# Optimization experiments

Hardware: AMD Instinct MI355X
Metric: run time of the kernel (lower is better)

The kernel has to match this reference:

```python
import jax, jax.numpy as jnp
import numpy as np
import functools

N_NODES = 16
WIDTH = 64
C_DIM = 3
LATENT_DIM = 8
B = 131072


def build_graph(n=N_NODES, k=4, p=0.75, seed=0):
    """Watts-Strogatz-style random graph oriented low->high node id (DAG),
    mirroring build_random_graph(nodes, 1 input, 1 output, p=0.75, k=4)."""
    rng = np.random.RandomState(seed)
    edges = set()
    for i in range(n):
        for d in range(1, k // 2 + 1):
            j = (i + d) % n
            if rng.rand() < p:
                j = int(rng.randint(n))
            a, b = min(i, j), max(i, j)
            if a != b:
                edges.add((a, b))
    preds = [set() for _ in range(n)]
    for a, b in edges:
        preds[b].add(a)
    # every non-source node must have a predecessor (connectivity)
    for j in range(1, n):
        if not preds[j]:
            a = int(rng.randint(j))
            preds[j].add(a)
            edges.add((a, j))
    succs = [set() for _ in range(n)]
    for a, b in edges:
        succs[a].add(b)
    preds = [sorted(p_) for p_ in preds]
    sources = [j for j in range(n) if not preds[j]]   # receive the INR feature f
    sinks = [j for j in range(n) if not succs[j]]     # combined into the single output
    return preds, sources, sinks


def gaussian(x):
    return jnp.exp(-0.5 * x * x)

# 'large' activation set for graph nodes, assigned deterministically per node
GRAPH_ACTS = [jnp.tanh, jax.nn.elu, jax.nn.softplus, jnp.sin, gaussian]


def setup_inputs() -> dict:
    key = jax.random.key(0)
    ks = jax.random.split(key, 16)

    def nrm(k, shape, s):
        return jax.random.normal(k, shape, dtype=jnp.float32) * s

    inputs = jax.random.normal(ks[0], (B, 3, 1), dtype=jnp.float32)   # (x, y, r) coords
    latents = jax.random.normal(ks[1], (B, LATENT_DIM), dtype=jnp.float32)
    Wl = nrm(ks[2], (WIDTH, LATENT_DIM), 0.3)
    bl = jnp.zeros((WIDTH,), jnp.float32)
    Wx = nrm(ks[3], (WIDTH, 1), 1.0)
    Wy = nrm(ks[4], (WIDTH, 1), 1.0)
    Wr = nrm(ks[5], (WIDTH, 1), 1.0)
    W1 = nrm(ks[6], (WIDTH, WIDTH), 0.15)
    b1 = jnp.zeros((WIDTH,), jnp.float32)
    gW = nrm(ks[7], (N_NODES, WIDTH, WIDTH), 0.15)   # per-graph-node Linear(width,width)
    gB = jnp.zeros((N_NODES, WIDTH), jnp.float32)
    outW = nrm(ks[8], (C_DIM, WIDTH), 0.15)          # combine -> c_dim output
    outb = jnp.zeros((C_DIM,), jnp.float32)
    scale = jnp.ones((1,), jnp.float32)              # ScaleAct learnable scalar
    return {"inputs": inputs, "latents": latents, "Wl": Wl, "bl": bl, "Wx": Wx,
            "Wy": Wy, "Wr": Wr, "W1": W1, "b1": b1, "gW": gW, "gB": gB,
            "outW": outW, "outb": outb, "scale": scale}


def reference(inputs, latents, Wl, bl, Wx, Wy, Wr, W1, b1, gW, gB, outW, outb, scale):
    x, y, r = inputs[:, 0, :], inputs[:, 1, :], inputs[:, 2, :]   # each (B, 1)
    latents_ = jnp.tanh(latents @ Wl.T + bl)      # acts_start[0] = Tanh
    r_ = jax.nn.elu(r @ Wr.T)                     # acts_start[1] = ELU
    y_ = jax.nn.softplus(y @ Wy.T)                # acts_start[2] = Softplus
    x_ = jnp.tanh(x @ Wx.T)                       # acts_start[3] = Tanh
    f = gaussian(x_ + y_ + r_ + latents_)         # acts_start[4] = Gaussian
    f = jnp.sin(f @ W1.T + b1)                    # acts_start[5] = SinLayer

    # random-topology graph network: gather(sum preds) -> linear -> activation
    preds, sources, sinks = build_graph()
    hs = []
    for j in range(N_NODES):
        if j in sources:
            inp = f
        else:
            inp = functools.reduce(lambda a, b_: a + b_, [hs[i] for i in preds[j]])
        hs.append(GRAPH_ACTS[j % len(GRAPH_ACTS)](inp @ gW[j].T + gB[j]))
    agg = functools.reduce(lambda a, b_: a + b_, [hs[j] for j in sinks])
    res = (agg @ outW.T + outb) * scale           # combine + ScaleAct
    return jax.nn.sigmoid(res)                    # final_activation='sigmoid'
```

## Files before the change

### kernel.cpp

```cpp
#include <hip/hip_runtime.h>
#include <cstdint>

#define NN 16
#define W64 64
#define MT 64
#define NSTAGE 17
#define IST 72
#define WST 68

typedef _Float16 half8   __attribute__((ext_vector_type(8)));
typedef _Float16 half16  __attribute__((ext_vector_type(16)));
typedef float    floatx4 __attribute__((ext_vector_type(4)));

struct GPlan {
    unsigned pred[NN];
    unsigned sinkmask;
    int slot[NSTAGE];
    int nslot;
};

constexpr unsigned mt_next(unsigned (&mt)[624], int &mti) {
    if (mti >= 624) {
        for (int i = 0; i < 624; ++i) {
            const unsigned y = (mt[i] & 0x80000000u) | (mt[(i + 1) % 624] & 0x7fffffffu);
            unsigned v = mt[(i + 397) % 624] ^ (y >> 1);
            if (y & 1u) v ^= 0x9908b0dfu;
            mt[i] = v;
        }
        mti = 0;
    }
    unsigned y = mt[mti++];
    y ^= y >> 11;
    y ^= (y << 7)  & 0x9d2c5680u;
    y ^= (y << 15) & 0xefc60000u;
    y ^= y >> 18;
    return y;
}
constexpr double mt_rnd(unsigned (&mt)[624], int &mti) {
    const unsigned a = mt_next(mt, mti) >> 5;
    const unsigned b = mt_next(mt, mti) >> 6;
    return (a * 67108864.0 + b) / 9007199254740992.0;
}
constexpr long mt_randint(unsigned (&mt)[624], int &mti, long n) {
    const unsigned long maxv = (unsigned long)n - 1;
    if (maxv == 0) return 0;
    unsigned long mask = maxv;
    mask |= mask >> 1;  mask |= mask >> 2;  mask |= mask >> 4;
    mask |= mask >> 8;  mask |= mask >> 16;
    unsigned long v = (unsigned long)mt_next(mt, mti) & mask;
    while (v > maxv) v = (unsigned long)mt_next(mt, mti) & mask;
    return (long)v;
}

constexpr GPlan build_plan() {
    GPlan P = {};
    unsigned mt[624] = {};
    mt[0] = 0u;
    for (int i = 1; i < 624; ++i)
        mt[i] = 1812433253u * (mt[i-1] ^ (mt[i-1] >> 30)) + (unsigned)i;
    int mti = 624;

    bool edge[NN][NN] = {};
    for (int i = 0; i < NN; ++i) {
        for (int d = 1; d <= 2; ++d) {
            int j = (i + d) & (NN - 1);
            if (mt_rnd(mt, mti) < 0.75) j = (int)mt_randint(mt, mti, NN);
            const int a = i < j ? i : j;
            const int b = i < j ? j : i;
            if (a != b) edge[a][b] = true;
        }
    }
    for (int a = 0; a < NN; ++a)
        for (int b = 0; b < NN; ++b)
            if (edge[a][b]) P.pred[b] |= 1u << a;
    for (int j = 1; j < NN; ++j) {
        if (!P.pred[j]) {
            const int a = (int)mt_randint(mt, mti, j);
            P.pred[j] |= 1u << a;
            edge[a][j] = true;
        }
    }
    unsigned succ[NN] = {};
    for (int a = 0; a < NN; ++a)
        for (int b = 0; b < NN; ++b)
            if (edge[a][b]) succ[a] |= 1u << b;
    for (int j = 0; j < NN; ++j)
        if (!succ[j]) P.sinkmask |= 1u << j;

    int lastuse[NSTAGE] = {};
    for (int v = 0; v < NSTAGE; ++v) lastuse[v] = -1;
    for (int j = 0; j < NN; ++j) {
        const unsigned pm = P.pred[j];
        if (pm == 0u) { if (j > lastuse[16]) lastuse[16] = j; }
        else for (int i = 0; i < NN; ++i)
            if (pm & (1u << i)) { if (j > lastuse[i]) lastuse[i] = j; }
    }
    for (int i = 0; i < NN; ++i)
        if (P.sinkmask & (1u << i)) lastuse[i] = 17;

    int defstage[NSTAGE] = {};
    for (int i = 0; i < NN; ++i) defstage[i] = i + 1;
    defstage[16] = 0;

    int nmax = 0;
    for (int s = 0; s <= 16; ++s) {
        const int w = (s == 0) ? 16 : (s - 1);
        bool busy[NSTAGE] = {};
        for (int v = 0; v < NSTAGE; ++v) {
            if (v == w) continue;
            if (defstage[v] < s && lastuse[v] >= s)
                busy[P.slot[v]] = true;
        }
        int k = 0;
        while (busy[k]) ++k;
        P.slot[w] = k;
        if (k + 1 > nmax) nmax = k + 1;
    }
    P.nslot = nmax;
    return P;
}

constexpr GPlan kPlan = build_plan();
constexpr int NSLOT = kPlan.nslot;

__device__ __forceinline__ float act_tanh(float x)     { return 1.0f - 2.0f / (1.0f + __expf(2.0f * x)); }
__device__ __forceinline__ float act_elu(float x)      { return x > 0.0f ? x : __expf(x) - 1.0f; }
__device__ __forceinline__ float act_softplus(float x) { return fmaxf(x, 0.0f) + __logf(1.0f + __expf(-fabsf(x))); }
__device__ __forceinline__ float act_gauss(float x)    { return __expf(-0.5f * x * x); }

__device__ __forceinline__ float apply_act(int a, float x) {
    switch (a) {
        case 0:  return act_tanh(x);
        case 1:  return act_elu(x);
        case 2:  return act_softplus(x);
        case 3:  return __sinf(x);
        default: return act_gauss(x);
    }
}

__device__ __forceinline__ half8 cvt8(float4 a, float4 b) {
    half8 h;
    h[0]=(_Float16)a.x; h[1]=(_Float16)a.y; h[2]=(_Float16)a.z; h[3]=(_Float16)a.w;
    h[4]=(_Float16)b.x; h[5]=(_Float16)b.y; h[6]=(_Float16)b.z; h[7]=(_Float16)b.w;
    return h;
}

__global__ void convert_weights(const float* __restrict__ W1,
                                const float* __restrict__ gW,
                                _Float16* __restrict__ ws)
{
    const int i = blockIdx.x * 256 + threadIdx.x;
    if (i >= NSTAGE * 4096) return;
    const float v = (i < 4096) ? W1[i] : gW[i - 4096];
    ws[i] = (_Float16)v;
}

template<bool F16W>
__global__ __launch_bounds__(256, 3) void inr_mfma_kernel(
    const float* __restrict__ inputs, const float* __restrict__ latents,
    const float* __restrict__ Wl, const float* __restrict__ bl,
    const float* __restrict__ Wx, const float* __restrict__ Wy,
    const float* __restrict__ Wr, const float* __restrict__ W1,
    const float* __restrict__ b1, const float* __restrict__ gW,
    const float* __restrict__ gB, const float* __restrict__ outW,
    const float* __restrict__ outb, const float* __restrict__ scale,
    const _Float16* __restrict__ wsW,
    float* __restrict__ out, int Btot)
{
    __shared__ __align__(16) _Float16 inpbuf[2][MT * IST];
    __shared__ __align__(16) _Float16 wbuf[W64 * WST];

    const int tid  = threadIdx.x;
    const int lane = tid & 63;
    const int wv   = tid >> 6;
    const int q    = lane >> 4;
    const int c    = lane & 15;
    const int rowbase = wv * 16;
    const int m0   = blockIdx.x * MT;

    const int srow = tid >> 3;
    const int sc8  = tid & 7;

    half16 hreg[NSLOT];

    {
        const int em = tid >> 2, ep = tid & 3;
        int mg = m0 + em; if (mg >= Btot) mg = Btot - 1;
        const float x = inputs[mg * 3 + 0];
        const float y = inputs[mg * 3 + 1];
        const float r = inputs[mg * 3 + 2];
        const float4 l0 = *(const float4*)(latents + mg * 8);
        const float4 l1 = *(const float4*)(latents + mg * 8 + 4);
        #pragma unroll
        for (int i = 0; i < 16; ++i) {
            const int k = ep * 16 + i;
            const float4 a = *(const float4*)(Wl + k * 8);
            const float4 b = *(const float4*)(Wl + k * 8 + 4);
            float ld = bl[k];
            ld = fmaf(l0.x, a.x, ld); ld = fmaf(l0.y, a.y, ld);
            ld = fmaf(l0.z, a.z, ld); ld = fmaf(l0.w, a.w, ld);
            ld = fmaf(l1.x, b.x, ld); ld = fmaf(l1.y, b.y, ld);
            ld = fmaf(l1.z, b.z, ld); ld = fmaf(l1.w, b.w, ld);
            const float tk = act_tanh(x * Wx[k]) + act_softplus(y * Wy[k])
                           + act_elu(r * Wr[k]) + act_tanh(ld);
            inpbuf[0][em * IST + k] = (_Float16)act_gauss(tk);
        }
    }
    if constexpr (F16W) {
        const uint4* src = (const uint4*)wsW;
        const uint4 h0 = src[tid], h1 = src[tid + 256];
        *(uint4*)&wbuf[srow * WST + sc8 * 8]        = h0;
        *(uint4*)&wbuf[(srow + 32) * WST + sc8 * 8] = h1;
    } else {
        const float4* src = (const float4*)W1;
        const float4 f0 = src[2 * tid],       f1 = src[2 * tid + 1];
        const float4 f2 = src[2 * tid + 512], f3 = src[2 * tid + 513];
        *(half8*)&wbuf[srow * WST + sc8 * 8]        = cvt8(f0, f1);
        *(half8*)&wbuf[(srow + 32) * WST + sc8 * 8] = cvt8(f2, f3);
    }
    __syncthreads();

    #pragma unroll
    for (int s = 0; s < NSTAGE; ++s) {
        const int slot = s & 1;

        uint4  nh0 = {}, nh1 = {};
        float4 nf0 = {}, nf1 = {}, nf2 = {}, nf3 = {};
        if (s + 1 < NSTAGE) {
            if constexpr (F16W) {
                const uint4* src = (const uint4*)(wsW + (s + 1) * 4096);
                nh0 = src[tid]; nh1 = src[tid + 256];
            } else {
                const float4* src = (const float4*)(gW + s * 4096);
                nf0 = src[2 * tid];       nf1 = src[2 * tid + 1];
                nf2 = src[2 * tid + 512]; nf3 = src[2 * tid + 513];
            }
        }

        const half8 a0 = *(const half8*)&inpbuf[slot][(rowbase + c) * IST +  0 + q * 8];
        const half8 a1 = *(const half8*)&inpbuf[slot][(rowbase + c) * IST + 32 + q * 8];

        const float* bias = (s == 0) ? b1 : (gB + (s - 1) * W64);
        floatx4 acc[4];
        #pragma unroll
        for (int t = 0; t < 4; ++t) {
            const half8 b0  = *(const half8*)&wbuf[(t * 16 + c) * WST +  0 + q * 8];
            const half8 b1f = *(const half8*)&wbuf[(t * 16 + c) * WST + 32 + q * 8];
            const float bs = bias[t * 16 + c];
            floatx4 z = {bs, bs, bs, bs};
            z = __builtin_amdgcn_mfma_f32_16x16x32_f16(a0, b0, z, 0, 0, 0);
            z = __builtin_amdgcn_mfma_f32_16x16x32_f16(a1, b1f, z, 0, 0, 0);
            acc[t] = z;
        }

        const int an    = (s == 0) ? 3 : ((s - 1) % 5);
        const int hslot = kPlan.slot[(s == 0) ? 16 : (s - 1)];
        #pragma unroll
        for (int t = 0; t < 4; ++t) {
            #pragma unroll
            for (int r = 0; r < 4; ++r) {
                const float v = apply_act(an, acc[t][r]);
                hreg[hslot][t * 4 + r] = (_Float16)v;
            }
        }

        if (s + 1 < NSTAGE) {
            const unsigned pm = kPlan.pred[s];
            half16 sum;
            if (pm == 0u) {
                sum = hreg[kPlan.slot[16]];
            } else {
                #pragma unroll
                for (int v = 0; v < 16; ++v) sum[v] = (_Float16)0.0f;
                #pragma unroll
                for (int i = 0; i < NN; ++i) {
                    if (pm & (1u << i)) {
                        sum += hreg[kPlan.slot[i]];
                    }
                }
            }
            const int wslot = (s + 1) & 1;
            #pragma unroll
            for (int t = 0; t < 4; ++t)
                #pragma unroll
                for (int r = 0; r < 4; ++r)
                    inpbuf[wslot][(rowbase + q * 4 + r) * IST + t * 16 + c] =
                        sum[t * 4 + r];

            __syncthreads();
            if constexpr (F16W) {
                *(uint4*)&wbuf[srow * WST + sc8 * 8]        = nh0;
                *(uint4*)&wbuf[(srow + 32) * WST + sc8 * 8] = nh1;
            } else {
                *(half8*)&wbuf[srow * WST + sc8 * 8]        = cvt8(nf0, nf1);
                *(half8*)&wbuf[(srow + 32) * WST + sc8 * 8] = cvt8(nf2, nf3);
            }
            __syncthreads();
        }
    }

    {
        half16 sum;
        #pragma unroll
        for (int v = 0; v < 16; ++v) sum[v] = (_Float16)0.0f;
        #pragma unroll
        for (int j = 0; j < NN; ++j) {
            if (kPlan.sinkmask & (1u << j)) {
                sum += hreg[kPlan.slot[j]];
            }
        }
        #pragma unroll
        for (int t = 0; t < 4; ++t)
            #pragma unroll
            for (int r = 0; r < 4; ++r)
                inpbuf[1][(rowbase + q * 4 + r) * IST + t * 16 + c] = sum[t * 4 + r];
    }
    {
        const int em = tid >> 2, ep = tid & 3;
        float p0 = 0.f, p1 = 0.f, p2 = 0.f;
        #pragma unroll
        for (int h = 0; h < 2; ++h) {
            const half8 hv = *(const half8*)&inpbuf[1][em * IST + ep * 16 + h * 8];
            #pragma unroll
            for (int i = 0; i < 8; ++i) {
                const float av = (float)hv[i];
                const int k = ep * 16 + h * 8 + i;
                p0 = fmaf(av, outW[0 * W64 + k], p0);
                p1 = fmaf(av, outW[1 * W64 + k], p1);
                p2 = fmaf(av, outW[2 * W64 + k], p2);
            }
        }
        p0 += __shfl_xor(p0, 1); p0 += __shfl_xor(p0, 2);
        p1 += __shfl_xor(p1, 1); p1 += __shfl_xor(p1, 2);
        p2 += __shfl_xor(p2, 1); p2 += __shfl_xor(p2, 2);
        const int mg = m0 + em;
        if (ep < 3 && mg < Btot) {
            const float pr = (ep == 0) ? p0 : ((ep == 1) ? p1 : p2);
            const float res = (pr + outb[ep]) * scale[0];
            out[mg * 3 + ep] = 1.0f / (1.0f + __expf(-res));
        }
    }
}

extern "C" void kernel_launch(void* const* d_in, const int* in_sizes, int n_in,
                              void* d_out, int out_size, void* d_ws, size_t ws_size,
                              hipStream_t stream)
{
    const float* inputs  = (const float*)d_in[0];
    const float* latents = (const float*)d_in[1];
    const float* Wl      = (const float*)d_in[2];
    const float* bl      = (const float*)d_in[3];
    const float* Wx      = (const float*)d_in[4];
    const float* Wy      = (const float*)d_in[5];
    const float* Wr      = (const float*)d_in[6];
    const float* W1      = (const float*)d_in[7];
    const float* b1      = (const float*)d_in[8];
    const float* gW      = (const float*)d_in[9];
    const float* gB      = (const float*)d_in[10];
    const float* outW    = (const float*)d_in[11];
    const float* outb    = (const float*)d_in[12];
    const float* scale   = (const float*)d_in[13];
    float* out = (float*)d_out;

    const int Btot = in_sizes[0] / 3;
    const int blocks = (Btot + MT - 1) / MT;
    const size_t wbytes = (size_t)NSTAGE * 4096 * sizeof(_Float16);

    if (ws_size >= wbytes) {
        _Float16* wsW = (_Float16*)d_ws;
        convert_weights<<<(NSTAGE * 4096 + 255) / 256, 256, 0, stream>>>(W1, gW, wsW);
        inr_mfma_kernel<true><<<blocks, 256, 0, stream>>>(
            inputs, latents, Wl, bl, Wx, Wy, Wr, W1, b1, gW, gB, outW, outb, scale,
            wsW, out, Btot);
    } else {
        inr_mfma_kernel<false><<<blocks, 256, 0, stream>>>(
            inputs, latents, Wl, bl, Wx, Wy, Wr, W1, b1, gW, gB, outW, outb, scale,
            (const _Float16*)nullptr, out, Btot);
    }
}
```

Measured before the change: 181.3 us.

## Transpose MFMA operands and read weights from global to drop block barriers

```diff
diff --git a/kernel.cpp b/kernel.cpp
--- a/kernel.cpp
+++ b/kernel.cpp
@@ -6,11 +6,12 @@
 #define MT 64
 #define NSTAGE 17
 #define IST 72
-#define WST 68
-
+
+typedef _Float16 half4   __attribute__((ext_vector_type(4)));
 typedef _Float16 half8   __attribute__((ext_vector_type(8)));
 typedef _Float16 half16  __attribute__((ext_vector_type(16)));
 typedef float    floatx4 __attribute__((ext_vector_type(4)));
+typedef unsigned int uint2v __attribute__((ext_vector_type(2)));
 
 struct GPlan {
     unsigned pred[NN];
@@ -156,7 +157,7 @@
 }
 
 template<bool F16W>
-__global__ __launch_bounds__(256, 3) void inr_mfma_kernel(
+__global__ __launch_bounds__(256, 4) void inr_mfma_kernel(
     const float* __restrict__ inputs, const float* __restrict__ latents,
     const float* __restrict__ Wl, const float* __restrict__ bl,
     const float* __restrict__ Wx, const float* __restrict__ Wy,
@@ -167,8 +168,7 @@
     const _Float16* __restrict__ wsW,
     float* __restrict__ out, int Btot)
 {
-    __shared__ __align__(16) _Float16 inpbuf[2][MT * IST];
-    __shared__ __align__(16) _Float16 wbuf[W64 * WST];
+    __shared__ __align__(16) _Float16 inpbuf[MT * IST];
 
     const int tid  = threadIdx.x;
     const int lane = tid & 63;
@@ -177,9 +177,6 @@
     const int c    = lane & 15;
     const int rowbase = wv * 16;
     const int m0   = blockIdx.x * MT;
-
-    const int srow = tid >> 3;
-    const int sc8  = tid & 7;
 
     half16 hreg[NSLOT];
 
@@ -191,6 +188,7 @@
         const float r = inputs[mg * 3 + 2];
         const float4 l0 = *(const float4*)(latents + mg * 8);
         const float4 l1 = *(const float4*)(latents + mg * 8 + 4);
+        half8 hlo, hhi;
         #pragma unroll
         for (int i = 0; i < 16; ++i) {
             const int k = ep * 16 + i;
@@ -203,53 +201,38 @@
             ld = fmaf(l1.z, b.z, ld); ld = fmaf(l1.w, b.w, ld);
             const float tk = act_tanh(x * Wx[k]) + act_softplus(y * Wy[k])
                            + act_elu(r * Wr[k]) + act_tanh(ld);
-            inpbuf[0][em * IST + k] = (_Float16)act_gauss(tk);
-        }
-    }
-    if constexpr (F16W) {
-        const uint4* src = (const uint4*)wsW;
-        const uint4 h0 = src[tid], h1 = src[tid + 256];
-        *(uint4*)&wbuf[srow * WST + sc8 * 8]        = h0;
-        *(uint4*)&wbuf[(srow + 32) * WST + sc8 * 8] = h1;
-    } else {
-        const float4* src = (const float4*)W1;
-        const float4 f0 = src[2 * tid],       f1 = src[2 * tid + 1];
-        const float4 f2 = src[2 * tid + 512], f3 = src[2 * tid + 513];
-        *(half8*)&wbuf[srow * WST + sc8 * 8]        = cvt8(f0, f1);
-        *(half8*)&wbuf[(srow + 32) * WST + sc8 * 8] = cvt8(f2, f3);
-    }
-    __syncthreads();
+            const _Float16 hv = (_Float16)act_gauss(tk);
+            if (i < 8) hlo[i] = hv; else hhi[i - 8] = hv;
+        }
+        *(half8*)&inpbuf[em * IST + ep * 16]     = hlo;
+        *(half8*)&inpbuf[em * IST + ep * 16 + 8] = hhi;
+    }
 
     #pragma unroll
     for (int s = 0; s < NSTAGE; ++s) {
-        const int slot = s & 1;
-
-        uint4  nh0 = {}, nh1 = {};
-        float4 nf0 = {}, nf1 = {}, nf2 = {}, nf3 = {};
-        if (s + 1 < NSTAGE) {
+        const half8 i0 = *(const half8*)&inpbuf[(rowbase + c) * IST +  0 + q * 8];
+        const half8 i1 = *(const half8*)&inpbuf[(rowbase + c) * IST + 32 + q * 8];
+
+        const float* bias = (s == 0) ? b1 : (gB + (s - 1) * W64);
+
+        floatx4 acc[4];
+        #pragma unroll
+        for (int t = 0; t < 4; ++t) {
+            half8 wlo, whi;
             if constexpr (F16W) {
-                const uint4* src = (const uint4*)(wsW + (s + 1) * 4096);
-                nh0 = src[tid]; nh1 = src[tid + 256];
+                const _Float16* wr = wsW + s * 4096 + (t * 16 + c) * 64 + q * 8;
+                wlo = *(const half8*)wr;
+                whi = *(const half8*)(wr + 32);
             } else {
-                const float4* src = (const float4*)(gW + s * 4096);
-                nf0 = src[2 * tid];       nf1 = src[2 * tid + 1];
-                nf2 = src[2 * tid + 512]; nf3 = src[2 * tid + 513];
-            }
-        }
-
-        const half8 a0 = *(const half8*)&inpbuf[slot][(rowbase + c) * IST +  0 + q * 8];
-        const half8 a1 = *(const half8*)&inpbuf[slot][(rowbase + c) * IST + 32 + q * 8];
-
-        const float* bias = (s == 0) ? b1 : (gB + (s - 1) * W64);
-        floatx4 acc[4];
-        #pragma unroll
-        for (int t = 0; t < 4; ++t) {
-            const half8 b0  = *(const half8*)&wbuf[(t * 16 + c) * WST +  0 + q * 8];
-            const half8 b1f = *(const half8*)&wbuf[(t * 16 + c) * WST + 32 + q * 8];
-            const float bs = bias[t * 16 + c];
-            floatx4 z = {bs, bs, bs, bs};
-            z = __builtin_amdgcn_mfma_f32_16x16x32_f16(a0, b0, z, 0, 0, 0);
-            z = __builtin_amdgcn_mfma_f32_16x16x32_f16(a1, b1f, z, 0, 0, 0);
+                const float* wr = ((s == 0) ? W1 : (gW + (s - 1) * 4096))
+                                  + (t * 16 + c) * 64 + q * 8;
+                wlo = cvt8(*(const float4*)wr,        *(const float4*)(wr + 4));
+                whi = cvt8(*(const float4*)(wr + 32), *(const float4*)(wr + 36));
+            }
+            const float4 bs = *(const float4*)(bias + t * 16 + q * 4);
+            floatx4 z = {bs.x, bs.y, bs.z, bs.w};
+            z = __builtin_amdgcn_mfma_f32_16x16x32_f16(wlo, i0, z, 0, 0, 0);
+            z = __builtin_amdgcn_mfma_f32_16x16x32_f16(whi, i1, z, 0, 0, 0);
             acc[t] = z;
         }
 
@@ -279,23 +262,10 @@
                     }
                 }
             }
-            const int wslot = (s + 1) & 1;
+            const uint2v* sp = (const uint2v*)&sum;
             #pragma unroll
             for (int t = 0; t < 4; ++t)
-                #pragma unroll
-                for (int r = 0; r < 4; ++r)
-                    inpbuf[wslot][(rowbase + q * 4 + r) * IST + t * 16 + c] =
-                        sum[t * 4 + r];
-
-            __syncthreads();
-            if constexpr (F16W) {
-                *(uint4*)&wbuf[srow * WST + sc8 * 8]        = nh0;
-                *(uint4*)&wbuf[(srow + 32) * WST + sc8 * 8] = nh1;
-            } else {
-                *(half8*)&wbuf[srow * WST + sc8 * 8]        = cvt8(nf0, nf1);
-                *(half8*)&wbuf[(srow + 32) * WST + sc8 * 8] = cvt8(nf2, nf3);
-            }
-            __syncthreads();
+                *(uint2v*)&inpbuf[(rowbase + c) * IST + t * 16 + q * 4] = sp[t];
         }
     }
 
@@ -309,35 +279,28 @@
                 sum += hreg[kPlan.slot[j]];
             }
         }
-        #pragma unroll
-        for (int t = 0; t < 4; ++t)
+        float p0 = 0.f, p1 = 0.f, p2 = 0.f;
+        #pragma unroll
+        for (int t = 0; t < 4; ++t) {
+            const float4 w0 = *(const float4*)(outW + 0 * W64 + t * 16 + q * 4);
+            const float4 w1 = *(const float4*)(outW + 1 * W64 + t * 16 + q * 4);
+            const float4 w2 = *(const float4*)(outW + 2 * W64 + t * 16 + q * 4);
             #pragma unroll
-            for (int r = 0; r < 4; ++r)
-                inpbuf[1][(rowbase + q * 4 + r) * IST + t * 16 + c] = sum[t * 4 + r];
-    }
-    {
-        const int em = tid >> 2, ep = tid & 3;
-        float p0 = 0.f, p1 = 0.f, p2 = 0.f;
-        #pragma unroll
-        for (int h = 0; h < 2; ++h) {
-            const half8 hv = *(const half8*)&inpbuf[1][em * IST + ep * 16 + h * 8];
-            #pragma unroll
-            for (int i = 0; i < 8; ++i) {
-                const float av = (float)hv[i];
-                const int k = ep * 16 + h * 8 + i;
-                p0 = fmaf(av, outW[0 * W64 + k], p0);
-                p1 = fmaf(av, outW[1 * W64 + k], p1);
-                p2 = fmaf(av, outW[2 * W64 + k], p2);
-            }
-        }
-        p0 += __shfl_xor(p0, 1); p0 += __shfl_xor(p0, 2);
-        p1 += __shfl_xor(p1, 1); p1 += __shfl_xor(p1, 2);
-        p2 += __shfl_xor(p2, 1); p2 += __shfl_xor(p2, 2);
-        const int mg = m0 + em;
-        if (ep < 3 && mg < Btot) {
-            const float pr = (ep == 0) ? p0 : ((ep == 1) ? p1 : p2);
-            const float res = (pr + outb[ep]) * scale[0];
-            out[mg * 3 + ep] = 1.0f / (1.0f + __expf(-res));
+            for (int r = 0; r < 4; ++r) {
+                const float av = (float)sum[t * 4 + r];
+                p0 = fmaf(av, ((const float*)&w0)[r], p0);
+                p1 = fmaf(av, ((const float*)&w1)[r], p1);
+                p2 = fmaf(av, ((const float*)&w2)[r], p2);
+            }
+        }
+        p0 += __shfl_xor(p0, 16); p0 += __shfl_xor(p0, 32);
+        p1 += __shfl_xor(p1, 16); p1 += __shfl_xor(p1, 32);
+        p2 += __shfl_xor(p2, 16); p2 += __shfl_xor(p2, 32);
+        const int mg = m0 + rowbase + c;
+        if (q < 3 && mg < Btot) {
+            const float pr  = (q == 0) ? p0 : ((q == 1) ? p1 : p2);
+            const float res = (pr + outb[q]) * scale[0];
+            out[mg * 3 + q] = 1.0f / (1.0f + __expf(-res));
         }
     }
 }
```

New measurement: 359.5 us. +98.4%, slower.
